# Optimization experiments

Hardware: AMD Instinct MI355X
Metric: run time of the kernel (lower is better)

Reference implementation:

```python
import jax, jax.numpy as jnp
import numpy as np

Q, N = 8, 256          # number of sub-networks, state dim per network
QN = Q * N             # 2048 total state dimension
BS = 128               # batch size
TMAX = 128             # time steps
STEP = 0.01            # Euler integration step size


def _offdiag_block_mask(q, n):
    # L_mask: ones everywhere except the q diagonal n x n blocks
    diag_blocks = np.kron(np.eye(q), np.ones((n, n)))
    return jnp.asarray(1.0 - diag_blocks, dtype=jnp.float32)


def setup_inputs() -> dict:
    key = jax.random.key(0)
    ks = jax.random.split(key, 6)
    s = 1.0 / np.sqrt(QN)  # keep 128-step Euler recurrence numerically tame
    X0 = jax.random.normal(ks[0], (BS, QN), dtype=jnp.float32)
    A = jax.random.normal(ks[1], (QN, QN), dtype=jnp.float32) * s
    B = jax.random.normal(ks[2], (QN, QN), dtype=jnp.float32) * s
    W = jax.random.normal(ks[3], (QN, QN), dtype=jnp.float32) * s
    # P is block-diagonal and well-conditioned (I + small block-diag noise)
    blk = np.kron(np.eye(Q), np.ones((N, N))).astype(np.float32)
    P = jnp.eye(QN, dtype=jnp.float32) + 0.1 * jax.random.normal(ks[4], (QN, QN), dtype=jnp.float32) * jnp.asarray(blk)
    bx = jax.random.normal(ks[5], (QN,), dtype=jnp.float32)
    return {"X0": X0, "A": A, "B": B, "W": W, "P": P, "bx": bx, "tmax": TMAX}


def reference(X0, A, B, W, P, bx, tmax):
    # mask GL weight to off-block-diagonal coupling, then L = W - P^{-1} W^T P
    Wm = W * _offdiag_block_mask(Q, N)
    L = Wm - jnp.linalg.solve(P, Wm.T @ P)
    M = A + L                      # (qn, qn)
    Xi0 = X0.T                     # (qn, bs)
    b = bx[:, None]                # (qn, 1) broadcast over batch

    def step_fn(Xi, _):
        Xn = Xi + STEP * (M @ Xi + B @ jax.nn.relu(Xi) + b)
        return Xn, Xn

    _, Xs = jax.lax.scan(step_fn, Xi0, None, length=tmax - 1)  # (tmax-1, qn, bs)
    X = jnp.concatenate([Xi0[None], Xs], axis=0)               # (tmax, qn, bs)
    return jnp.transpose(X, (2, 0, 1))                          # (bs, tmax, qn)
```

## Files before the change

### kernel.cpp

```cpp
#include <hip/hip_runtime.h>

typedef unsigned short u16;
typedef __attribute__((ext_vector_type(8))) short bf16x8;
typedef __attribute__((ext_vector_type(4))) float f32x4;
typedef __attribute__((ext_vector_type(4))) unsigned short u16x4;

#define QN    2048
#define BSZ   128
#define TMAXK 128
#define STEPF 0.01f
#define NEWTON_ITERS 46

__device__ __forceinline__ u16 f2bf(float f){
  unsigned u = __float_as_uint(f);
  u += 0x7fffu + ((u >> 16) & 1u);
  return (u16)(u >> 16);
}
__device__ __forceinline__ float bf2f(u16 h){
  return __uint_as_float(((unsigned)h) << 16);
}


__global__ __launch_bounds__(256) void alpha_k(const float* __restrict__ P, float* __restrict__ alpha){
  int q = blockIdx.x, i = threadIdx.x;
  const float* Pb = P + (size_t)(q << 8) * QN + (q << 8);
  float rs = 0.f, cs = 0.f;
  for (int c = 0; c < 256; ++c){
    rs += fabsf(Pb[(size_t)i * QN + c]);
    cs += fabsf(Pb[(size_t)c * QN + i]);
  }
  __shared__ float red[256];
  red[i] = rs; __syncthreads();
  for (int o = 128; o > 0; o >>= 1){ if (i < o) red[i] = fmaxf(red[i], red[i+o]); __syncthreads(); }
  float mr = red[0];
  __syncthreads();
  red[i] = cs; __syncthreads();
  for (int o = 128; o > 0; o >>= 1){ if (i < o) red[i] = fmaxf(red[i], red[i+o]); __syncthreads(); }
  if (i == 0) alpha[q] = mr * red[0];
}

__global__ __launch_bounds__(256) void initV_k(const float* __restrict__ P, const float* __restrict__ alpha, float* __restrict__ V){
  int idx = blockIdx.x * 256 + threadIdx.x;
  int q = idx >> 16, rc = idx & 65535;
  int r = rc >> 8, c = rc & 255;
  V[idx] = P[(size_t)((q << 8) + c) * QN + (q << 8) + r] / alpha[q];
}

__global__ __launch_bounds__(256) void newton_T_k(const float* __restrict__ P, const float* __restrict__ Vin, float* __restrict__ Tm){
  int q = blockIdx.x >> 4;
  int tl = blockIdx.x & 15;
  int rb = (tl >> 2) << 6, cb = (tl & 3) << 6;
  const float* Ab = P + (size_t)(q << 8) * QN + (q << 8);
  const float* Bb = Vin + (q << 16);
  __shared__ float Asm[16][68];
  __shared__ float Bsm[16][68];
  int tid = threadIdx.x, ty = tid >> 4, tx = tid & 15;
  float acc[4][4];
#pragma unroll
  for (int i = 0; i < 4; i++)
#pragma unroll
    for (int j = 0; j < 4; j++) acc[i][j] = 0.f;
  int ar = tid >> 2, ak = (tid & 3) << 2;
  int bc = tid & 63, bk = tid >> 6;
  for (int kb = 0; kb < 256; kb += 16){
    f32x4 av = *(const f32x4*)(Ab + (size_t)(rb + ar) * QN + kb + ak);
    float b0 = Bb[(size_t)(kb + bk     ) * 256 + cb + bc];
    float b1 = Bb[(size_t)(kb + bk +  4) * 256 + cb + bc];
    float b2 = Bb[(size_t)(kb + bk +  8) * 256 + cb + bc];
    float b3 = Bb[(size_t)(kb + bk + 12) * 256 + cb + bc];
    __syncthreads();
    Asm[ak+0][ar] = av.x; Asm[ak+1][ar] = av.y; Asm[ak+2][ar] = av.z; Asm[ak+3][ar] = av.w;
    Bsm[bk   ][bc] = b0;  Bsm[bk+ 4][bc] = b1;  Bsm[bk+ 8][bc] = b2;  Bsm[bk+12][bc] = b3;
    __syncthreads();
#pragma unroll
    for (int kk = 0; kk < 16; kk++){
      f32x4 a = *(const f32x4*)&Asm[kk][ty << 2];
      f32x4 b = *(const f32x4*)&Bsm[kk][tx << 2];
#pragma unroll
      for (int i = 0; i < 4; i++)
#pragma unroll
        for (int j = 0; j < 4; j++) acc[i][j] += a[i] * b[j];
    }
  }
  float* Ob = Tm + (q << 16);
#pragma unroll
  for (int i = 0; i < 4; i++){
    f32x4 o; o.x = acc[i][0]; o.y = acc[i][1]; o.z = acc[i][2]; o.w = acc[i][3];
    *(f32x4*)(Ob + (size_t)(rb + (ty << 2) + i) * 256 + cb + (tx << 2)) = o;
  }
}

__global__ __launch_bounds__(256) void newton_V_k(const float* __restrict__ Vin, const float* __restrict__ Tm, float* __restrict__ Vout){
  int q = blockIdx.x >> 4;
  int tl = blockIdx.x & 15;
  int rb = (tl >> 2) << 6, cb = (tl & 3) << 6;
  const float* Ab = Vin + (q << 16);
  const float* Bb = Tm + (q << 16);
  __shared__ float Asm[16][68];
  __shared__ float Bsm[16][68];
  int tid = threadIdx.x, ty = tid >> 4, tx = tid & 15;
  float acc[4][4];
#pragma unroll
  for (int i = 0; i < 4; i++)
#pragma unroll
    for (int j = 0; j < 4; j++) acc[i][j] = 0.f;
  int ar = tid >> 2, ak = (tid & 3) << 2;
  int bc = tid & 63, bk = tid >> 6;
  for (int kb = 0; kb < 256; kb += 16){
    f32x4 av = *(const f32x4*)(Ab + (size_t)(rb + ar) * 256 + kb + ak);
    float b0 = Bb[(size_t)(kb + bk     ) * 256 + cb + bc];
    float b1 = Bb[(size_t)(kb + bk +  4) * 256 + cb + bc];
    float b2 = Bb[(size_t)(kb + bk +  8) * 256 + cb + bc];
    float b3 = Bb[(size_t)(kb + bk + 12) * 256 + cb + bc];
    __syncthreads();
    Asm[ak+0][ar] = av.x; Asm[ak+1][ar] = av.y; Asm[ak+2][ar] = av.z; Asm[ak+3][ar] = av.w;
    Bsm[bk   ][bc] = b0;  Bsm[bk+ 4][bc] = b1;  Bsm[bk+ 8][bc] = b2;  Bsm[bk+12][bc] = b3;
    __syncthreads();
#pragma unroll
    for (int kk = 0; kk < 16; kk++){
      f32x4 a = *(const f32x4*)&Asm[kk][ty << 2];
      f32x4 b = *(const f32x4*)&Bsm[kk][tx << 2];
#pragma unroll
      for (int i = 0; i < 4; i++)
#pragma unroll
        for (int j = 0; j < 4; j++) acc[i][j] += a[i] * b[j];
    }
  }
  float* Ob = Vout + (q << 16);
#pragma unroll
  for (int i = 0; i < 4; i++){
    f32x4 vo = *(const f32x4*)(Ab + (size_t)(rb + (ty << 2) + i) * 256 + cb + (tx << 2));
    f32x4 o;
    o.x = 2.f*vo.x - acc[i][0]; o.y = 2.f*vo.y - acc[i][1];
    o.z = 2.f*vo.z - acc[i][2]; o.w = 2.f*vo.w - acc[i][3];
    *(f32x4*)(Ob + (size_t)(rb + (ty << 2) + i) * 256 + cb + (tx << 2)) = o;
  }
}

__global__ __launch_bounds__(256) void build_Y_k(const float* __restrict__ W, const float* __restrict__ P, float* __restrict__ Ymat){
  int j  = blockIdx.x >> 7;
  int rt = (blockIdx.x >> 2) & 31;
  int ct = blockIdx.x & 3;
  int rb = rt << 6, cb = ct << 6, jb = j << 8;
  int tid = threadIdx.x, ty = tid >> 4, tx = tid & 15;
  if ((rt >> 2) == j){
#pragma unroll
    for (int i = 0; i < 4; i++){
      f32x4 z = {0.f, 0.f, 0.f, 0.f};
      *(f32x4*)(Ymat + (size_t)(rb + (ty << 2) + i) * QN + jb + cb + (tx << 2)) = z;
    }
    return;
  }
  __shared__ float Asm[16][68];
  __shared__ float Bsm[16][68];
  float acc[4][4];
#pragma unroll
  for (int i = 0; i < 4; i++)
#pragma unroll
    for (int j2 = 0; j2 < 4; j2++) acc[i][j2] = 0.f;
  int sr = tid & 63, sk = tid >> 6;
  for (int kb = 0; kb < 256; kb += 16){
    float a0 = W[(size_t)(jb + kb + sk     ) * QN + rb + sr];
    float a1 = W[(size_t)(jb + kb + sk +  4) * QN + rb + sr];
    float a2 = W[(size_t)(jb + kb + sk +  8) * QN + rb + sr];
    float a3 = W[(size_t)(jb + kb + sk + 12) * QN + rb + sr];
    float b0 = P[(size_t)(jb + kb + sk     ) * QN + jb + cb + sr];
    float b1 = P[(size_t)(jb + kb + sk +  4) * QN + jb + cb + sr];
    float b2 = P[(size_t)(jb + kb + sk +  8) * QN + jb + cb + sr];
    float b3 = P[(size_t)(jb + kb + sk + 12) * QN + jb + cb + sr];
    __syncthreads();
    Asm[sk   ][sr] = a0; Asm[sk+ 4][sr] = a1; Asm[sk+ 8][sr] = a2; Asm[sk+12][sr] = a3;
    Bsm[sk   ][sr] = b0; Bsm[sk+ 4][sr] = b1; Bsm[sk+ 8][sr] = b2; Bsm[sk+12][sr] = b3;
    __syncthreads();
#pragma unroll
    for (int kk = 0; kk < 16; kk++){
      f32x4 a = *(const f32x4*)&Asm[kk][ty << 2];
      f32x4 b = *(const f32x4*)&Bsm[kk][tx << 2];
#pragma unroll
      for (int i = 0; i < 4; i++)
#pragma unroll
        for (int j2 = 0; j2 < 4; j2++) acc[i][j2] += a[i] * b[j2];
    }
  }
#pragma unroll
  for (int i = 0; i < 4; i++){
    f32x4 o; o.x = acc[i][0]; o.y = acc[i][1]; o.z = acc[i][2]; o.w = acc[i][3];
    *(f32x4*)(Ymat + (size_t)(rb + (ty << 2) + i) * QN + jb + cb + (tx << 2)) = o;
  }
}

__global__ __launch_bounds__(256) void build_C_k(const float* __restrict__ Vfin, const float* __restrict__ Ymat,
                                                 const float* __restrict__ Ain, const float* __restrict__ W,
                                                 u16* __restrict__ C1, u16* __restrict__ C2){
  int ib = blockIdx.x >> 7;
  int rest = blockIdx.x & 127;
  int rt = rest >> 5, ct = rest & 31;
  int rb = rt << 6, cb = ct << 6;
  const float* Ab = Vfin + (ib << 16);
  __shared__ float Asm[16][68];
  __shared__ float Bsm[16][68];
  int tid = threadIdx.x, ty = tid >> 4, tx = tid & 15;
  float acc[4][4];
#pragma unroll
  for (int i = 0; i < 4; i++)
#pragma unroll
    for (int j = 0; j < 4; j++) acc[i][j] = 0.f;
  int ar = tid >> 2, ak = (tid & 3) << 2;
  int bc = tid & 63, bk = tid >> 6;
  for (int kb = 0; kb < 256; kb += 16){
    f32x4 av = *(const f32x4*)(Ab + (size_t)(rb + ar) * 256 + kb + ak);
    float b0 = Ymat[(size_t)((ib << 8) + kb + bk     ) * QN + cb + bc];
    float b1 = Ymat[(size_t)((ib << 8) + kb + bk +  4) * QN + cb + bc];
    float b2 = Ymat[(size_t)((ib << 8) + kb + bk +  8) * QN + cb + bc];
    float b3 = Ymat[(size_t)((ib << 8) + kb + bk + 12) * QN + cb + bc];
    __syncthreads();
    Asm[ak+0][ar] = av.x; Asm[ak+1][ar] = av.y; Asm[ak+2][ar] = av.z; Asm[ak+3][ar] = av.w;
    Bsm[bk   ][bc] = b0;  Bsm[bk+ 4][bc] = b1;  Bsm[bk+ 8][bc] = b2;  Bsm[bk+12][bc] = b3;
    __syncthreads();
#pragma unroll
    for (int kk = 0; kk < 16; kk++){
      f32x4 a = *(const f32x4*)&Asm[kk][ty << 2];
      f32x4 b = *(const f32x4*)&Bsm[kk][tx << 2];
#pragma unroll
      for (int i = 0; i < 4; i++)
#pragma unroll
        for (int j = 0; j < 4; j++) acc[i][j] += a[i] * b[j];
    }
  }
#pragma unroll
  for (int i = 0; i < 4; i++){
    int row = (ib << 8) + rb + (ty << 2) + i;
#pragma unroll
    for (int j = 0; j < 4; j++){
      int col = cb + (tx << 2) + j;
      float wv = ((row >> 8) == (col >> 8)) ? 0.f : W[(size_t)row * QN + col];
      float m = Ain[(size_t)row * QN + col] + wv - acc[i][j];
      u16 hi = f2bf(m);
      u16 lo = f2bf(m - bf2f(hi));
      C1[((size_t)row << 12) + col] = hi;
      C2[((size_t)row << 12) + col] = lo;
    }
  }
}

__global__ __launch_bounds__(256) void split_B_k(const float* __restrict__ Bin, u16* __restrict__ C1, u16* __restrict__ C2){
  int idx = blockIdx.x * 256 + threadIdx.x;
  int r = idx >> 11, c = idx & 2047;
  float v = Bin[idx];
  u16 hi = f2bf(v);
  u16 lo = f2bf(v - bf2f(hi));
  C1[((size_t)r << 12) + 2048 + c] = hi;
  C2[((size_t)r << 12) + 2048 + c] = lo;
}

__global__ __launch_bounds__(256) void init_state_k(const float* __restrict__ X0, float* __restrict__ Xf,
                                                    u16* __restrict__ Yst, float* __restrict__ out){
  int idx = blockIdx.x * 256 + threadIdx.x;
  int bs = idx >> 11, qn = idx & 2047;
  float x = X0[idx];
  Xf[idx] = x;
  Yst[((size_t)bs << 12) + qn] = f2bf(x);
  Yst[((size_t)bs << 12) + 2048 + qn] = f2bf(fmaxf(x, 0.f));
  out[((size_t)bs * TMAXK) * QN + qn] = x;
}


__global__ __launch_bounds__(256) void step_gemm_k(const u16* __restrict__ C1, const u16* __restrict__ C2,
                                                   const u16* __restrict__ Yst, float* __restrict__ part){
  __shared__ __align__(16) char lds[65536];
  int tid = threadIdx.x;
  int rg = blockIdx.x >> 4, s = blockIdx.x & 15;
  int k0 = s << 8;
  for (int ro = 0; ro < 16; ++ro){
    int e = ro * 256 + tid;
    const u16* src = (e < 2048) ? C1 : C2;
    int el = e & 2047;
    int r = el >> 5;
    int k8 = (el & 31) << 3;
    bf16x8 v = *(const bf16x8*)(src + ((size_t)((rg << 6) + r) << 12) + k0 + k8);
    int addr = ((e >> 11) << 15) + ((((r << 9) + (k8 << 1))) ^ ((r & 7) << 4));
    *(bf16x8*)(lds + addr) = v;
  }
  __syncthreads();
  int w = tid >> 6, l = tid & 63;
  int lo16 = l & 15, hi = l >> 4;
  f32x4 acc[4][2];
#pragma unroll
  for (int m = 0; m < 4; m++)
#pragma unroll
    for (int n = 0; n < 2; n++){ acc[m][n].x = 0.f; acc[m][n].y = 0.f; acc[m][n].z = 0.f; acc[m][n].w = 0.f; }
  const u16* yb = Yst + ((size_t)((w << 5) + lo16) << 12) + k0 + (hi << 3);
#pragma unroll
  for (int ks = 0; ks < 8; ++ks){
    bf16x8 b0 = *(const bf16x8*)(yb + ks * 32);
    bf16x8 b1 = *(const bf16x8*)(yb + 65536 + ks * 32);
    int kb2 = (ks * 32 + (hi << 3)) << 1;
#pragma unroll
    for (int m = 0; m < 4; m++){
      int row = (m << 4) + lo16;
      int ba = ((row << 9) + kb2) ^ ((row & 7) << 4);
      bf16x8 a1 = *(const bf16x8*)(lds + ba);
      bf16x8 a2 = *(const bf16x8*)(lds + 32768 + ba);
      acc[m][0] = __builtin_amdgcn_mfma_f32_16x16x32_bf16(a1, b0, acc[m][0], 0, 0, 0);
      acc[m][0] = __builtin_amdgcn_mfma_f32_16x16x32_bf16(a2, b0, acc[m][0], 0, 0, 0);
      acc[m][1] = __builtin_amdgcn_mfma_f32_16x16x32_bf16(a1, b1, acc[m][1], 0, 0, 0);
      acc[m][1] = __builtin_amdgcn_mfma_f32_16x16x32_bf16(a2, b1, acc[m][1], 0, 0, 0);
    }
  }
#pragma unroll
  for (int m = 0; m < 4; m++)
#pragma unroll
    for (int n = 0; n < 2; n++){
      int bs = (w << 5) + (n << 4) + lo16;
      int row = (rg << 6) + (m << 4) + (hi << 2);
      *(f32x4*)(part + ((size_t)(s * BSZ + bs) << 11) + row) = acc[m][n];
    }
}

__global__ __launch_bounds__(256) void step_update_k(const float* __restrict__ part, float* __restrict__ Xf,
                                                     const float* __restrict__ bx, u16* __restrict__ Yst,
                                                     float* __restrict__ out, int t){
  int tid = blockIdx.x * 256 + threadIdx.x;
  int bs = tid >> 9;
  int row = (tid & 511) << 2;
  size_t base = ((size_t)bs << 11) + row;
  f32x4 u = {0.f, 0.f, 0.f, 0.f};
#pragma unroll
  for (int s = 0; s < 16; s++){
    f32x4 p = *(const f32x4*)(part + ((size_t)s << 18) + base);
    u += p;
  }
  f32x4 x = *(const f32x4*)(Xf + base);
  f32x4 b = *(const f32x4*)(bx + row);
  f32x4 xn = x + STEPF * (u + b);
  *(f32x4*)(Xf + base) = xn;
  *(f32x4*)(out + ((size_t)(bs * TMAXK + t) << 11) + row) = xn;
  u16x4 hv, rv;
  hv.x = f2bf(xn.x); hv.y = f2bf(xn.y); hv.z = f2bf(xn.z); hv.w = f2bf(xn.w);
  rv.x = f2bf(fmaxf(xn.x, 0.f)); rv.y = f2bf(fmaxf(xn.y, 0.f));
  rv.z = f2bf(fmaxf(xn.z, 0.f)); rv.w = f2bf(fmaxf(xn.w, 0.f));
  *(u16x4*)(Yst + ((size_t)bs << 12) + row) = hv;
  *(u16x4*)(Yst + ((size_t)bs << 12) + 2048 + row) = rv;
}


extern "C" void kernel_launch(void* const* d_in, const int* in_sizes, int n_in,
                              void* d_out, int out_size, void* d_ws, size_t ws_size,
                              hipStream_t stream){
  (void)in_sizes; (void)n_in; (void)out_size; (void)ws_size;
  const float* X0  = (const float*)d_in[0];
  const float* Ain = (const float*)d_in[1];
  const float* Bin = (const float*)d_in[2];
  const float* Win = (const float*)d_in[3];
  const float* Pin = (const float*)d_in[4];
  const float* bx  = (const float*)d_in[5];
  float* out = (float*)d_out;
  char* ws = (char*)d_ws;
  const size_t MB = 1u << 20;

  u16*   C1    = (u16*)(ws);
  u16*   C2    = (u16*)(ws + 16*MB);
  float* Xf    = (float*)(ws + 32*MB);
  u16*   Yst   = (u16*)(ws + 33*MB);
  float* Ymat  = (float*)(ws + 34*MB);
  float* part  = (float*)(ws + 34*MB);
  float* Vb0   = (float*)(ws + 50*MB);
  float* Vb1   = (float*)(ws + 52*MB);
  float* Tm    = (float*)(ws + 54*MB);
  float* alpha = (float*)(ws + 56*MB);

  alpha_k<<<8, 256, 0, stream>>>(Pin, alpha);
  initV_k<<<2048, 256, 0, stream>>>(Pin, alpha, Vb0);
  float* Vc = Vb0; float* Vo = Vb1;
  for (int it = 0; it < NEWTON_ITERS; ++it){
    newton_T_k<<<128, 256, 0, stream>>>(Pin, Vc, Tm);
    newton_V_k<<<128, 256, 0, stream>>>(Vc, Tm, Vo);
    float* tmp = Vc; Vc = Vo; Vo = tmp;
  }
  build_Y_k<<<1024, 256, 0, stream>>>(Win, Pin, Ymat);
  build_C_k<<<1024, 256, 0, stream>>>(Vc, Ymat, Ain, Win, C1, C2);
  split_B_k<<<16384, 256, 0, stream>>>(Bin, C1, C2);
  init_state_k<<<1024, 256, 0, stream>>>(X0, Xf, Yst, out);

  for (int t = 1; t < TMAXK; ++t){
    step_gemm_k<<<512, 256, 0, stream>>>(C1, C2, Yst, part);
    step_update_k<<<256, 256, 0, stream>>>(part, Xf, bx, Yst, out, t);
  }
}
```

Baseline: 3.811 ms.

## Fuse time-step loop into persistent cooperative kernel with grid barriers

Replaces the 254 per-step GEMM and update launches with one cooperative persistent kernel of 256 blocks. Each block loads its 64-row by 512-K slice of the hi/lo weight matrices into 128KB of LDS once and keeps it there for all steps. Two grid-wide atomic barriers per step separate the partial-sum GEMM from the reduction and state update, and the state is carried in registers. This removes launch overhead and the per-step weight reloads from global memory, at the cost of barrier latency and one block per CU.

```diff
diff --git a/kernel.cpp b/kernel.cpp
--- a/kernel.cpp
+++ b/kernel.cpp
@@ -3,13 +3,14 @@
 typedef unsigned short u16;
 typedef __attribute__((ext_vector_type(8))) short bf16x8;
 typedef __attribute__((ext_vector_type(4))) float f32x4;
-typedef __attribute__((ext_vector_type(4))) unsigned short u16x4;
+typedef __attribute__((ext_vector_type(2))) float f32x2;
 
 #define QN    2048
 #define BSZ   128
 #define TMAXK 128
 #define STEPF 0.01f
 #define NEWTON_ITERS 46
+#define NBLK  256
 
 __device__ __forceinline__ u16 f2bf(float f){
   unsigned u = __float_as_uint(f);
@@ -253,94 +254,105 @@
   C2[((size_t)r << 12) + 2048 + c] = lo;
 }
 
-__global__ __launch_bounds__(256) void init_state_k(const float* __restrict__ X0, float* __restrict__ Xf,
+__global__ __launch_bounds__(256) void init_state_k(const float* __restrict__ X0,
                                                     u16* __restrict__ Yst, float* __restrict__ out){
   int idx = blockIdx.x * 256 + threadIdx.x;
   int bs = idx >> 11, qn = idx & 2047;
   float x = X0[idx];
-  Xf[idx] = x;
   Yst[((size_t)bs << 12) + qn] = f2bf(x);
   Yst[((size_t)bs << 12) + 2048 + qn] = f2bf(fmaxf(x, 0.f));
   out[((size_t)bs * TMAXK) * QN + qn] = x;
 }
 
 
-__global__ __launch_bounds__(256) void step_gemm_k(const u16* __restrict__ C1, const u16* __restrict__ C2,
-                                                   const u16* __restrict__ Yst, float* __restrict__ part){
-  __shared__ __align__(16) char lds[65536];
-  int tid = threadIdx.x;
-  int rg = blockIdx.x >> 4, s = blockIdx.x & 15;
-  int k0 = s << 8;
-  for (int ro = 0; ro < 16; ++ro){
-    int e = ro * 256 + tid;
-    const u16* src = (e < 2048) ? C1 : C2;
-    int el = e & 2047;
-    int r = el >> 5;
-    int k8 = (el & 31) << 3;
-    bf16x8 v = *(const bf16x8*)(src + ((size_t)((rg << 6) + r) << 12) + k0 + k8);
-    int addr = ((e >> 11) << 15) + ((((r << 9) + (k8 << 1))) ^ ((r & 7) << 4));
+__device__ __forceinline__ void grid_bar(unsigned* cnt, unsigned* gen, unsigned target){
+  __syncthreads();
+  if (threadIdx.x == 0){
+    __threadfence();
+    unsigned old = __hip_atomic_fetch_add(cnt, 1u, __ATOMIC_ACQ_REL, __HIP_MEMORY_SCOPE_AGENT);
+    if (old == (unsigned)(NBLK - 1)){
+      __hip_atomic_store(cnt, 0u, __ATOMIC_RELAXED, __HIP_MEMORY_SCOPE_AGENT);
+      __hip_atomic_store(gen, target, __ATOMIC_RELEASE, __HIP_MEMORY_SCOPE_AGENT);
+    } else {
+      while (__hip_atomic_load(gen, __ATOMIC_ACQUIRE, __HIP_MEMORY_SCOPE_AGENT) < target)
+        __builtin_amdgcn_s_sleep(2);
+    }
+    __threadfence();
+  }
+  __syncthreads();
+}
+
+__global__ void __launch_bounds__(512, 1) persist_k(
+    const u16* __restrict__ C1, const u16* __restrict__ C2,
+    u16* __restrict__ Yst, float* __restrict__ part,
+    const float* __restrict__ X0, const float* __restrict__ bx,
+    float* __restrict__ out, unsigned* cnt, unsigned* gen){
+  extern __shared__ char lds[];
+  int b = blockIdx.x, tid = threadIdx.x;
+  int rg = b >> 3, s = b & 7;
+  for (int it = 0; it < 16; ++it){
+    int e = it * 512 + tid;
+    const u16* src = (e < 4096) ? C1 : C2;
+    int el = e & 4095;
+    int r = el >> 6;
+    int k8 = (el & 63) << 3;
+    bf16x8 v = *(const bf16x8*)(src + ((size_t)((rg << 6) + r) << 12) + (s << 9) + k8);
+    int addr = ((e >> 12) << 16) + ((((r << 10) + (k8 << 1))) ^ ((r & 7) << 4));
     *(bf16x8*)(lds + addr) = v;
   }
   __syncthreads();
   int w = tid >> 6, l = tid & 63;
   int lo16 = l & 15, hi = l >> 4;
-  f32x4 acc[4][2];
-#pragma unroll
-  for (int m = 0; m < 4; m++)
-#pragma unroll
-    for (int n = 0; n < 2; n++){ acc[m][n].x = 0.f; acc[m][n].y = 0.f; acc[m][n].z = 0.f; acc[m][n].w = 0.f; }
-  const u16* yb = Yst + ((size_t)((w << 5) + lo16) << 12) + k0 + (hi << 3);
-#pragma unroll
-  for (int ks = 0; ks < 8; ++ks){
-    bf16x8 b0 = *(const bf16x8*)(yb + ks * 32);
-    bf16x8 b1 = *(const bf16x8*)(yb + 65536 + ks * 32);
-    int kb2 = (ks * 32 + (hi << 3)) << 1;
-#pragma unroll
-    for (int m = 0; m < 4; m++){
-      int row = (m << 4) + lo16;
-      int ba = ((row << 9) + kb2) ^ ((row & 7) << 4);
+  int m = w & 3, nh = w >> 2;
+  int row16 = (m << 4) + lo16;
+  int abase = ((row16 << 10)) ^ ((row16 & 7) << 4);
+  const u16* yb0 = Yst + ((size_t)((nh << 6) + lo16) << 12) + (s << 9) + (hi << 3);
+  int g = b * 512 + tid;
+  int bs_u = g >> 10;
+  int row2 = (g & 1023) << 1;
+  size_t xbase = ((size_t)bs_u << 11) + row2;
+  float b0v = bx[row2], b1v = bx[row2 + 1];
+  float x0 = X0[xbase], x1 = X0[xbase + 1];
+  unsigned bt = 0;
+  for (int t = 1; t < TMAXK; ++t){
+    f32x4 acc[4];
+#pragma unroll
+    for (int n = 0; n < 4; n++) acc[n] = (f32x4){0.f, 0.f, 0.f, 0.f};
+#pragma unroll 4
+    for (int ks = 0; ks < 16; ++ks){
+      int ba = abase + ((ks << 6) + (hi << 4)) ;
+      ba = ((row16 << 10) + ((ks << 6) + (hi << 4))) ^ ((row16 & 7) << 4);
       bf16x8 a1 = *(const bf16x8*)(lds + ba);
-      bf16x8 a2 = *(const bf16x8*)(lds + 32768 + ba);
-      acc[m][0] = __builtin_amdgcn_mfma_f32_16x16x32_bf16(a1, b0, acc[m][0], 0, 0, 0);
-      acc[m][0] = __builtin_amdgcn_mfma_f32_16x16x32_bf16(a2, b0, acc[m][0], 0, 0, 0);
-      acc[m][1] = __builtin_amdgcn_mfma_f32_16x16x32_bf16(a1, b1, acc[m][1], 0, 0, 0);
-      acc[m][1] = __builtin_amdgcn_mfma_f32_16x16x32_bf16(a2, b1, acc[m][1], 0, 0, 0);
-    }
-  }
-#pragma unroll
-  for (int m = 0; m < 4; m++)
-#pragma unroll
-    for (int n = 0; n < 2; n++){
-      int bs = (w << 5) + (n << 4) + lo16;
+      bf16x8 a2 = *(const bf16x8*)(lds + 65536 + ba);
+#pragma unroll
+      for (int n = 0; n < 4; ++n){
+        bf16x8 bf = *(const bf16x8*)(yb0 + ((size_t)n << 16) + (ks << 5));
+        acc[n] = __builtin_amdgcn_mfma_f32_16x16x32_bf16(a1, bf, acc[n], 0, 0, 0);
+        acc[n] = __builtin_amdgcn_mfma_f32_16x16x32_bf16(a2, bf, acc[n], 0, 0, 0);
+      }
+    }
+#pragma unroll
+    for (int n = 0; n < 4; ++n){
+      int bs = (nh << 6) + (n << 4) + lo16;
       int row = (rg << 6) + (m << 4) + (hi << 2);
-      *(f32x4*)(part + ((size_t)(s * BSZ + bs) << 11) + row) = acc[m][n];
-    }
-}
-
-__global__ __launch_bounds__(256) void step_update_k(const float* __restrict__ part, float* __restrict__ Xf,
-                                                     const float* __restrict__ bx, u16* __restrict__ Yst,
-                                                     float* __restrict__ out, int t){
-  int tid = blockIdx.x * 256 + threadIdx.x;
-  int bs = tid >> 9;
-  int row = (tid & 511) << 2;
-  size_t base = ((size_t)bs << 11) + row;
-  f32x4 u = {0.f, 0.f, 0.f, 0.f};
-#pragma unroll
-  for (int s = 0; s < 16; s++){
-    f32x4 p = *(const f32x4*)(part + ((size_t)s << 18) + base);
-    u += p;
-  }
-  f32x4 x = *(const f32x4*)(Xf + base);
-  f32x4 b = *(const f32x4*)(bx + row);
-  f32x4 xn = x + STEPF * (u + b);
-  *(f32x4*)(Xf + base) = xn;
-  *(f32x4*)(out + ((size_t)(bs * TMAXK + t) << 11) + row) = xn;
-  u16x4 hv, rv;
-  hv.x = f2bf(xn.x); hv.y = f2bf(xn.y); hv.z = f2bf(xn.z); hv.w = f2bf(xn.w);
-  rv.x = f2bf(fmaxf(xn.x, 0.f)); rv.y = f2bf(fmaxf(xn.y, 0.f));
-  rv.z = f2bf(fmaxf(xn.z, 0.f)); rv.w = f2bf(fmaxf(xn.w, 0.f));
-  *(u16x4*)(Yst + ((size_t)bs << 12) + row) = hv;
-  *(u16x4*)(Yst + ((size_t)bs << 12) + 2048 + row) = rv;
+      *(f32x4*)(part + ((size_t)((s << 7) + bs) << 11) + row) = acc[n];
+    }
+    grid_bar(cnt, gen, ++bt);
+    float u0 = 0.f, u1 = 0.f;
+#pragma unroll
+    for (int sl = 0; sl < 8; ++sl){
+      const float* pp = part + ((size_t)((sl << 7) + bs_u) << 11) + row2;
+      u0 += pp[0]; u1 += pp[1];
+    }
+    x0 = x0 + STEPF * (u0 + b0v);
+    x1 = x1 + STEPF * (u1 + b1v);
+    *(f32x2*)(out + ((size_t)((bs_u << 7) + t) << 11) + row2) = (f32x2){x0, x1};
+    unsigned hv = (unsigned)f2bf(x0) | ((unsigned)f2bf(x1) << 16);
+    unsigned rv = (unsigned)f2bf(fmaxf(x0, 0.f)) | ((unsigned)f2bf(fmaxf(x1, 0.f)) << 16);
+    *(unsigned*)(Yst + ((size_t)bs_u << 12) + row2) = hv;
+    *(unsigned*)(Yst + ((size_t)bs_u << 12) + 2048 + row2) = rv;
+    grid_bar(cnt, gen, ++bt);
+  }
 }
 
 
@@ -358,16 +370,19 @@
   char* ws = (char*)d_ws;
   const size_t MB = 1u << 20;
 
-  u16*   C1    = (u16*)(ws);
-  u16*   C2    = (u16*)(ws + 16*MB);
-  float* Xf    = (float*)(ws + 32*MB);
-  u16*   Yst   = (u16*)(ws + 33*MB);
-  float* Ymat  = (float*)(ws + 34*MB);
-  float* part  = (float*)(ws + 34*MB);
-  float* Vb0   = (float*)(ws + 50*MB);
-  float* Vb1   = (float*)(ws + 52*MB);
-  float* Tm    = (float*)(ws + 54*MB);
-  float* alpha = (float*)(ws + 56*MB);
+  u16*     C1    = (u16*)(ws);
+  u16*     C2    = (u16*)(ws + 16*MB);
+  unsigned* barc = (unsigned*)(ws + 32*MB);
+  unsigned* barg = (unsigned*)(ws + 32*MB + 256);
+  u16*     Yst   = (u16*)(ws + 33*MB);
+  float*   Ymat  = (float*)(ws + 34*MB);
+  float*   part  = (float*)(ws + 34*MB);
+  float*   Vb0   = (float*)(ws + 50*MB);
+  float*   Vb1   = (float*)(ws + 52*MB);
+  float*   Tm    = (float*)(ws + 54*MB);
+  float*   alpha = (float*)(ws + 56*MB);
+
+  hipMemsetAsync(ws + 32*MB, 0, 512, stream);
 
   alpha_k<<<8, 256, 0, stream>>>(Pin, alpha);
   initV_k<<<2048, 256, 0, stream>>>(Pin, alpha, Vb0);
@@ -380,10 +395,10 @@
   build_Y_k<<<1024, 256, 0, stream>>>(Win, Pin, Ymat);
   build_C_k<<<1024, 256, 0, stream>>>(Vc, Ymat, Ain, Win, C1, C2);
   split_B_k<<<16384, 256, 0, stream>>>(Bin, C1, C2);
-  init_state_k<<<1024, 256, 0, stream>>>(X0, Xf, Yst, out);
-
-  for (int t = 1; t < TMAXK; ++t){
-    step_gemm_k<<<512, 256, 0, stream>>>(C1, C2, Yst, part);
-    step_update_k<<<256, 256, 0, stream>>>(part, Xf, bx, Yst, out, t);
-  }
-}
+  init_state_k<<<1024, 256, 0, stream>>>(X0, Yst, out);
+
+  hipFuncSetAttribute((const void*)persist_k, hipFuncAttributeMaxDynamicSharedMemorySize, 131072);
+  void* kargs[] = {(void*)&C1, (void*)&C2, (void*)&Yst, (void*)&part,
+                   (void*)&X0, (void*)&bx, (void*)&out, (void*)&barc, (void*)&barg};
+  hipLaunchCooperativeKernel((void*)persist_k, dim3(NBLK), dim3(512), kargs, 131072, stream);
+}
```

Result: slower. 11.55 ms (+203.0%).
